# Kernel tuning notes

Hardware: AMD Instinct MI355X
Metric: run time of the kernel (lower is better)

The kernel has to match this reference:

```python
import jax, jax.numpy as jnp
from jax import lax
import numpy as np

B = 1024
CH = 32          # decomp.channel
LEVEL = 3        # decomp.level
CTOT = CH * (LEVEL + 1)   # 128, ODE state dim == GRU input dim
T_POINTS = 96    # decomp.eval_time_points
PRED_LEN = 96
HID = 128


def _dopri5_traj(y0, ts, Wo, bo):
    """Fixed-grid Dormand-Prince 5(4) integration of dy/dt = tanh(y Wo^T + bo).
    y0: [B, CTOT]; ts: [T]. Returns trajectory [T, B, CTOT]."""
    f = lambda y: jnp.tanh(y @ Wo.T + bo)

    def step(y, dt):
        k1 = f(y)
        k2 = f(y + dt * (0.2 * k1))
        k3 = f(y + dt * (3.0 / 40 * k1 + 9.0 / 40 * k2))
        k4 = f(y + dt * (44.0 / 45 * k1 - 56.0 / 15 * k2 + 32.0 / 9 * k3))
        k5 = f(y + dt * (19372.0 / 6561 * k1 - 25360.0 / 2187 * k2 + 64448.0 / 6561 * k3 - 212.0 / 729 * k4))
        k6 = f(y + dt * (9017.0 / 3168 * k1 - 355.0 / 33 * k2 + 46732.0 / 5247 * k3 + 49.0 / 176 * k4 - 5103.0 / 18656 * k5))
        y_next = y + dt * (35.0 / 384 * k1 + 500.0 / 1113 * k3 + 125.0 / 192 * k4 - 2187.0 / 6784 * k5 + 11.0 / 84 * k6)
        return y_next, y_next

    _, ys = lax.scan(step, y0, ts[1:] - ts[:-1])
    return jnp.concatenate([y0[None], ys], axis=0)


def _gru_layer(xs, W_ih, W_hh, b_ih, b_hh):
    """PyTorch-semantics GRU layer. xs: [T, B, D] -> hidden states [T, B, H]."""
    gi = jnp.einsum('tbd,gd->tbg', xs, W_ih) + b_ih  # precompute input gates
    H = W_hh.shape[1]

    def cell(h, gi_t):
        gh = h @ W_hh.T + b_hh
        i_r, i_z, i_n = jnp.split(gi_t, 3, axis=-1)
        h_r, h_z, h_n = jnp.split(gh, 3, axis=-1)
        r = jax.nn.sigmoid(i_r + h_r)
        z = jax.nn.sigmoid(i_z + h_z)
        n = jnp.tanh(i_n + r * h_n)
        h_new = (1.0 - z) * n + z * h
        return h_new, h_new

    h0 = jnp.zeros((xs.shape[1], H), xs.dtype)
    _, hs = lax.scan(cell, h0, gi)
    return hs


def setup_inputs() -> dict:
    key = jax.random.key(0)
    ks = jax.random.split(key, 20)
    s = 0.08  # ~1/sqrt(128), keeps GRU/ODE in a stable regime
    return {
        'x': jax.random.normal(ks[0], (B, CH, 256), jnp.float32),
        'yl': jax.random.normal(ks[1], (B, CH, 1), jnp.float32),
        'yh': jax.random.normal(ks[2], (B, CH * LEVEL, 1), jnp.float32),
        'W_ode': jax.random.normal(ks[3], (CTOT, CTOT), jnp.float32) * 0.05,
        'b_ode': jax.random.normal(ks[4], (CTOT,), jnp.float32) * 0.05,
        'W_ih0': jax.random.normal(ks[5], (3 * HID, CTOT), jnp.float32) * s,
        'W_hh0': jax.random.normal(ks[6], (3 * HID, HID), jnp.float32) * s,
        'b_ih0': jax.random.normal(ks[7], (3 * HID,), jnp.float32) * s,
        'b_hh0': jax.random.normal(ks[8], (3 * HID,), jnp.float32) * s,
        'W_ih1': jax.random.normal(ks[9], (3 * HID, HID), jnp.float32) * s,
        'W_hh1': jax.random.normal(ks[10], (3 * HID, HID), jnp.float32) * s,
        'b_ih1': jax.random.normal(ks[11], (3 * HID,), jnp.float32) * s,
        'b_hh1': jax.random.normal(ks[12], (3 * HID,), jnp.float32) * s,
        'W1': jax.random.normal(ks[13], (64, HID), jnp.float32) * s,
        'b1': jax.random.normal(ks[14], (64,), jnp.float32) * s,
        'W2': jax.random.normal(ks[15], (PRED_LEN * CH, 64), jnp.float32) * 0.125,
        'b2': jax.random.normal(ks[16], (PRED_LEN * CH,), jnp.float32) * 0.125,
    }


def reference(x, yl, yh, W_ode, b_ode,
              W_ih0, W_hh0, b_ih0, b_hh0,
              W_ih1, W_hh1, b_ih1, b_hh1,
              W1, b1, W2, b2):
    # coeffs = cat([yl] + yh, dim=1) -> [B, CTOT, 1] -> squeeze coeff length (=1)
    coeffs = jnp.concatenate([yl, yh], axis=1)[..., 0]  # [B, CTOT]
    ts = jnp.linspace(0.0, 1.0, T_POINTS)
    traj = _dopri5_traj(coeffs, ts, W_ode, b_ode)  # [T, B, CTOT]
    # rearrange 't b c l -> b t (c l)' with l == 1; GRU scans over leading T axis
    h1 = _gru_layer(traj, W_ih0, W_hh0, b_ih0, b_hh0)   # [T, B, HID]
    h2 = _gru_layer(h1, W_ih1, W_hh1, b_ih1, b_hh1)     # [T, B, HID]
    last = h2[-1]                                        # [B, HID]
    hidden = jax.nn.gelu(last @ W1.T + b1, approximate=False)
    pred = hidden @ W2.T + b2                            # [B, PRED_LEN*CH]
    return pred.reshape(-1, CH, PRED_LEN)
```

## Files before the change

### kernel.cpp

```cpp
#include <hip/hip_runtime.h>
#include <hip/hip_bf16.h>
#include <math.h>

#define ROWS 16
#define NTHR 512
#define TPTS 96
#define CTOT 128
#define NBLK 64

typedef __bf16 bf16x8_t __attribute__((ext_vector_type(8)));
typedef float f32x4_t __attribute__((ext_vector_type(4)));
typedef unsigned short us8_t __attribute__((ext_vector_type(8)));

__device__ __forceinline__ unsigned short f2b(float f) {
    union { float f; unsigned int i; } v; v.f = f;
    unsigned int r = v.i + 0x7fffu + ((v.i >> 16) & 1u);
    return (unsigned short)(r >> 16);
}
__device__ __forceinline__ f32x4_t mfma16(bf16x8_t a, bf16x8_t b, f32x4_t c) {
    return __builtin_amdgcn_mfma_f32_16x16x32_bf16(a, b, c, 0, 0, 0);
}
__device__ __forceinline__ bf16x8_t ldfrag(const unsigned short* p) {
    us8_t v = *(const us8_t*)p;
    return __builtin_bit_cast(bf16x8_t, v);
}
__device__ __forceinline__ bf16x8_t ldfrag_f32(const float* p) {
    bf16x8_t r;
#pragma unroll
    for (int j = 0; j < 8; ++j) {
        unsigned short us = f2b(p[j]);
        r[j] = __builtin_bit_cast(__bf16, us);
    }
    return r;
}
__device__ __forceinline__ float tanh_fast(float x) {
    float xc = fminf(fmaxf(x, -20.f), 20.f);
    float ez = __expf(-2.f * xc);
    return __fdividef(1.f - ez, 1.f + ez);
}
__device__ __forceinline__ float sigm(float x) {
    return __fdividef(1.f, 1.f + __expf(-x));
}

__global__ void __launch_bounds__(NTHR)
ode_forecaster(const float* __restrict__ yl,
               const float* __restrict__ yh,
               const float* __restrict__ Wode,
               const float* __restrict__ bode,
               const float* __restrict__ Wih0,
               const float* __restrict__ Whh0,
               const float* __restrict__ bih0,
               const float* __restrict__ bhh0,
               const float* __restrict__ Wih1,
               const float* __restrict__ Whh1,
               const float* __restrict__ bih1,
               const float* __restrict__ bhh1,
               const float* __restrict__ W1v,
               const float* __restrict__ b1v,
               const float* __restrict__ W2v,
               const float* __restrict__ b2v,
               float* __restrict__ outp,
               unsigned short* __restrict__ traj)
{
    const int tid  = threadIdx.x;
    const int lane = tid & 63;
    const int wv   = tid >> 6;
    const int l15  = lane & 15;
    const int quad = lane >> 4;
    const int r0   = blockIdx.x * ROWS;
    const int row0 = quad * 4;
    const int u    = wv * 16 + l15;

    __shared__ __align__(16) unsigned short hbuf[2][ROWS * 136];
    __shared__ __align__(16) unsigned short hidbuf[ROWS * 72];

    unsigned short* trajB = traj + (size_t)blockIdx.x * (TPTS * ROWS * CTOT);

    float y[4];
#pragma unroll
    for (int i = 0; i < 4; ++i) {
        int R = r0 + row0 + i;
        y[i] = (u < 32) ? yl[R * 32 + u] : yh[R * 96 + (u - 32)];
        unsigned short yb = f2b(y[i]);
        hbuf[0][(row0 + i) * 136 + u] = yb;
        trajB[(size_t)0 + (row0 + i) * CTOT + u] = yb;
    }

    bf16x8_t wode[4];
#pragma unroll
    for (int kt = 0; kt < 4; ++kt)
        wode[kt] = ldfrag_f32(Wode + u * 128 + kt * 32 + quad * 8);
    const float bo = bode[u];

    __syncthreads();

    const float dt = 1.0f / 95.0f;
    const float DA1_0 = 0.2f;
    const float DA2_0 = 3.f / 40.f, DA2_1 = 9.f / 40.f;
    const float DA3_0 = 44.f / 45.f, DA3_1 = -56.f / 15.f, DA3_2 = 32.f / 9.f;
    const float DA4_0 = 19372.f / 6561.f, DA4_1 = -25360.f / 2187.f,
                DA4_2 = 64448.f / 6561.f, DA4_3 = -212.f / 729.f;
    const float DA5_0 = 9017.f / 3168.f, DA5_1 = -355.f / 33.f,
                DA5_2 = 46732.f / 5247.f, DA5_3 = 49.f / 176.f, DA5_4 = -5103.f / 18656.f;
    const float B1 = 35.f / 384.f, B3 = 500.f / 1113.f, B4 = 125.f / 192.f,
                B5 = -2187.f / 6784.f, B6 = 11.f / 84.f;

    int p = 0;
    float kr[6][4];
#pragma unroll 1
    for (int t = 0; t < 95; ++t) {
#pragma unroll
        for (int s = 0; s < 6; ++s) {
            bf16x8_t af[4];
#pragma unroll
            for (int kt = 0; kt < 4; ++kt)
                af[kt] = ldfrag(&hbuf[p][l15 * 136 + kt * 32 + quad * 8]);
            f32x4_t acc = {0.f, 0.f, 0.f, 0.f};
#pragma unroll
            for (int kt = 0; kt < 4; ++kt) acc = mfma16(af[kt], wode[kt], acc);
#pragma unroll
            for (int i = 0; i < 4; ++i) kr[s][i] = tanh_fast(acc[i] + bo);

            if (s < 5) {
#pragma unroll
                for (int i = 0; i < 4; ++i) {
                    float zv = 0.f;
                    if (s == 0) { zv = DA1_0 * kr[0][i]; }
                    else if (s == 1) { zv = DA2_0 * kr[0][i] + DA2_1 * kr[1][i]; }
                    else if (s == 2) { zv = DA3_0 * kr[0][i] + DA3_1 * kr[1][i] + DA3_2 * kr[2][i]; }
                    else if (s == 3) { zv = DA4_0 * kr[0][i] + DA4_1 * kr[1][i] + DA4_2 * kr[2][i] + DA4_3 * kr[3][i]; }
                    else { zv = DA5_0 * kr[0][i] + DA5_1 * kr[1][i] + DA5_2 * kr[2][i] + DA5_3 * kr[3][i] + DA5_4 * kr[4][i]; }
                    hbuf[p ^ 1][(row0 + i) * 136 + u] = f2b(y[i] + dt * zv);
                }
            } else {
#pragma unroll
                for (int i = 0; i < 4; ++i) {
                    float fc = B1 * kr[0][i] + B3 * kr[2][i] + B4 * kr[3][i] + B5 * kr[4][i] + B6 * kr[5][i];
                    y[i] += dt * fc;
                    unsigned short yb = f2b(y[i]);
                    hbuf[p ^ 1][(row0 + i) * 136 + u] = yb;
                    trajB[(size_t)(t + 1) * (ROWS * CTOT) + (row0 + i) * CTOT + u] = yb;
                }
            }
            __syncthreads();
            p ^= 1;
        }
    }

    const float* WihL[2] = {Wih0, Wih1};
    const float* WhhL[2] = {Whh0, Whh1};
    const float* bihL[2] = {bih0, bih1};
    const float* bhhL[2] = {bhh0, bhh1};

    float h[4];
#pragma unroll 1
    for (int layer = 0; layer < 2; ++layer) {
        const float* Wih = WihL[layer];
        const float* Whh = WhhL[layer];
        bf16x8_t wih[3][4], whh[3][4];
#pragma unroll
        for (int g = 0; g < 3; ++g) {
            int nrow = g * 128 + u;
#pragma unroll
            for (int kt = 0; kt < 4; ++kt) {
                wih[g][kt] = ldfrag_f32(Wih + nrow * 128 + kt * 32 + quad * 8);
                whh[g][kt] = ldfrag_f32(Whh + nrow * 128 + kt * 32 + quad * 8);
            }
        }
        const float bir  = bihL[layer][u];
        const float biz  = bihL[layer][128 + u];
        const float bin_ = bihL[layer][256 + u];
        const float bhr  = bhhL[layer][u];
        const float bhz  = bhhL[layer][128 + u];
        const float bhn  = bhhL[layer][256 + u];

#pragma unroll
        for (int i = 0; i < 4; ++i) h[i] = 0.f;
        p = 0;
        for (int idx = tid; idx < ROWS * 136; idx += NTHR) hbuf[0][idx] = 0;
        __syncthreads();

#pragma unroll 1
        for (int t = 0; t < TPTS; ++t) {
            if (layer == 0 && t > 0) {
#pragma unroll
                for (int i = 0; i < 4; ++i)
                    trajB[(size_t)(t - 1) * (ROWS * CTOT) + (row0 + i) * CTOT + u] = f2b(h[i]);
            }
            const unsigned short* xp = trajB + (size_t)t * (ROWS * CTOT) + l15 * CTOT;
            bf16x8_t ax[4], ah[4];
#pragma unroll
            for (int kt = 0; kt < 4; ++kt) ax[kt] = ldfrag(xp + kt * 32 + quad * 8);
#pragma unroll
            for (int kt = 0; kt < 4; ++kt)
                ah[kt] = ldfrag(&hbuf[p][l15 * 136 + kt * 32 + quad * 8]);

            f32x4_t gi0 = {0.f,0.f,0.f,0.f}, gi1 = {0.f,0.f,0.f,0.f}, gi2 = {0.f,0.f,0.f,0.f};
            f32x4_t gh0 = {0.f,0.f,0.f,0.f}, gh1 = {0.f,0.f,0.f,0.f}, gh2 = {0.f,0.f,0.f,0.f};
#pragma unroll
            for (int kt = 0; kt < 4; ++kt) {
                gi0 = mfma16(ax[kt], wih[0][kt], gi0);
                gi1 = mfma16(ax[kt], wih[1][kt], gi1);
                gi2 = mfma16(ax[kt], wih[2][kt], gi2);
                gh0 = mfma16(ah[kt], whh[0][kt], gh0);
                gh1 = mfma16(ah[kt], whh[1][kt], gh1);
                gh2 = mfma16(ah[kt], whh[2][kt], gh2);
            }
#pragma unroll
            for (int i = 0; i < 4; ++i) {
                float rr = sigm((gi0[i] + bir) + (gh0[i] + bhr));
                float zz = sigm((gi1[i] + biz) + (gh1[i] + bhz));
                float nn = tanh_fast((gi2[i] + bin_) + rr * (gh2[i] + bhn));
                h[i] = (1.f - zz) * nn + zz * h[i];
                hbuf[p ^ 1][(row0 + i) * 136 + u] = f2b(h[i]);
            }
            __syncthreads();
            p ^= 1;
        }
        if (layer == 0) {
#pragma unroll
            for (int i = 0; i < 4; ++i)
                trajB[(size_t)95 * (ROWS * CTOT) + (row0 + i) * CTOT + u] = f2b(h[i]);
        }
    }

    if (wv < 4) {
        bf16x8_t a4[4], bw[4];
#pragma unroll
        for (int kt = 0; kt < 4; ++kt) {
            a4[kt] = ldfrag(&hbuf[p][l15 * 136 + kt * 32 + quad * 8]);
            bw[kt] = ldfrag_f32(W1v + (wv * 16 + l15) * 128 + kt * 32 + quad * 8);
        }
        f32x4_t acc = {0.f, 0.f, 0.f, 0.f};
#pragma unroll
        for (int kt = 0; kt < 4; ++kt) acc = mfma16(a4[kt], bw[kt], acc);
        const float bb = b1v[wv * 16 + l15];
#pragma unroll
        for (int i = 0; i < 4; ++i) {
            float x = acc[i] + bb;
            float g = 0.5f * x * (1.0f + erff(x * 0.70710678118654752f));
            hidbuf[(row0 + i) * 72 + wv * 16 + l15] = f2b(g);
        }
    }
    __syncthreads();

    bf16x8_t ahid[2];
#pragma unroll
    for (int kt = 0; kt < 2; ++kt)
        ahid[kt] = ldfrag(&hidbuf[l15 * 72 + kt * 32 + quad * 8]);
#pragma unroll 1
    for (int j = 0; j < 24; ++j) {
        int n = (wv * 24 + j) * 16 + l15;
        bf16x8_t bb0 = ldfrag_f32(W2v + n * 64 + quad * 8);
        bf16x8_t bb1 = ldfrag_f32(W2v + n * 64 + 32 + quad * 8);
        f32x4_t acc = {0.f, 0.f, 0.f, 0.f};
        acc = mfma16(ahid[0], bb0, acc);
        acc = mfma16(ahid[1], bb1, acc);
        const float bv = b2v[n];
#pragma unroll
        for (int i = 0; i < 4; ++i)
            outp[(size_t)(r0 + row0 + i) * 3072 + n] = acc[i] + bv;
    }
}

extern "C" void kernel_launch(void* const* d_in, const int* in_sizes, int n_in,
                              void* d_out, int out_size, void* d_ws, size_t ws_size,
                              hipStream_t stream) {
    const float* yl   = (const float*)d_in[1];
    const float* yh   = (const float*)d_in[2];
    const float* Wode = (const float*)d_in[3];
    const float* bode = (const float*)d_in[4];
    const float* Wih0 = (const float*)d_in[5];
    const float* Whh0 = (const float*)d_in[6];
    const float* bih0 = (const float*)d_in[7];
    const float* bhh0 = (const float*)d_in[8];
    const float* Wih1 = (const float*)d_in[9];
    const float* Whh1 = (const float*)d_in[10];
    const float* bih1 = (const float*)d_in[11];
    const float* bhh1 = (const float*)d_in[12];
    const float* W1v  = (const float*)d_in[13];
    const float* b1v  = (const float*)d_in[14];
    const float* W2v  = (const float*)d_in[15];
    const float* b2v  = (const float*)d_in[16];

    ode_forecaster<<<dim3(NBLK), dim3(NTHR), 0, stream>>>(
        yl, yh, Wode, bode, Wih0, Whh0, bih0, bhh0,
        Wih1, Whh1, bih1, bhh1, W1v, b1v, W2v, b2v,
        (float*)d_out, (unsigned short*)d_ws);
}
```

Measured before the change: 834.2 us.

## Split fused ODE-GRU kernel into ODE, input-gate GEMM, and recurrent GRU kernels

The single fused kernel is replaced by five launches. An ODE kernel processes 32 rows per block, a fully parallel kernel precomputes the GRU input gates for all timesteps, and a recurrent GRU kernel handles only the hidden-to-hidden matmul, prefetching gate values two steps ahead. This takes the input projection off the serial critical path and gives each block two independent MFMA chains. The cost is halving the recurrent grid to 32 blocks, which leaves most of the GPU idle, plus large global workspace traffic for the bf16-packed gate tensors. It also adds packed bf16 conversions, vectorized loads and a cheaper tanh.

```diff
diff --git a/kernel.cpp b/kernel.cpp
--- a/kernel.cpp
+++ b/kernel.cpp
@@ -2,11 +2,9 @@
 #include <hip/hip_bf16.h>
 #include <math.h>
 
-#define ROWS 16
-#define NTHR 512
 #define TPTS 96
 #define CTOT 128
-#define NBLK 64
+#define LDP 134
 
 typedef __bf16 bf16x8_t __attribute__((ext_vector_type(8)));
 typedef float f32x4_t __attribute__((ext_vector_type(4)));
@@ -17,6 +15,24 @@
     unsigned int r = v.i + 0x7fffu + ((v.i >> 16) & 1u);
     return (unsigned short)(r >> 16);
 }
+__device__ __forceinline__ unsigned int packbf2(float a, float b) {
+#if __has_builtin(__builtin_amdgcn_cvt_pk_bf16_f32)
+    typedef __bf16 bf16x2_t __attribute__((ext_vector_type(2)));
+    bf16x2_t v = __builtin_amdgcn_cvt_pk_bf16_f32(a, b);
+    return __builtin_bit_cast(unsigned int, v);
+#else
+    return (unsigned int)f2b(a) | ((unsigned int)f2b(b) << 16);
+#endif
+}
+__device__ __forceinline__ uint2 pack4(float v0, float v1, float v2, float v3) {
+    uint2 w; w.x = packbf2(v0, v1); w.y = packbf2(v2, v3); return w;
+}
+__device__ __forceinline__ float u2f_lo(unsigned int w) {
+    union { unsigned int i; float f; } v; v.i = w << 16; return v.f;
+}
+__device__ __forceinline__ float u2f_hi(unsigned int w) {
+    union { unsigned int i; float f; } v; v.i = w & 0xffff0000u; return v.f;
+}
 __device__ __forceinline__ f32x4_t mfma16(bf16x8_t a, bf16x8_t b, f32x4_t c) {
     return __builtin_amdgcn_mfma_f32_16x16x32_bf16(a, b, c, 0, 0, 0);
 }
@@ -24,242 +40,317 @@
     us8_t v = *(const us8_t*)p;
     return __builtin_bit_cast(bf16x8_t, v);
 }
-__device__ __forceinline__ bf16x8_t ldfrag_f32(const float* p) {
+__device__ __forceinline__ bf16x8_t ldfragW(const float* p) {
+    float4 a = *(const float4*)p;
+    float4 b = *(const float4*)(p + 4);
     bf16x8_t r;
-#pragma unroll
-    for (int j = 0; j < 8; ++j) {
-        unsigned short us = f2b(p[j]);
-        r[j] = __builtin_bit_cast(__bf16, us);
-    }
+    r[0] = __builtin_bit_cast(__bf16, f2b(a.x)); r[1] = __builtin_bit_cast(__bf16, f2b(a.y));
+    r[2] = __builtin_bit_cast(__bf16, f2b(a.z)); r[3] = __builtin_bit_cast(__bf16, f2b(a.w));
+    r[4] = __builtin_bit_cast(__bf16, f2b(b.x)); r[5] = __builtin_bit_cast(__bf16, f2b(b.y));
+    r[6] = __builtin_bit_cast(__bf16, f2b(b.z)); r[7] = __builtin_bit_cast(__bf16, f2b(b.w));
     return r;
 }
-__device__ __forceinline__ float tanh_fast(float x) {
-    float xc = fminf(fmaxf(x, -20.f), 20.f);
-    float ez = __expf(-2.f * xc);
-    return __fdividef(1.f - ez, 1.f + ez);
+__device__ __forceinline__ float tanh2(float x) {
+    float e = __expf(x + x);
+    return 1.f - __fdividef(2.f, e + 1.f);
 }
 __device__ __forceinline__ float sigm(float x) {
     return __fdividef(1.f, 1.f + __expf(-x));
 }
 
-__global__ void __launch_bounds__(NTHR)
-ode_forecaster(const float* __restrict__ yl,
-               const float* __restrict__ yh,
-               const float* __restrict__ Wode,
-               const float* __restrict__ bode,
-               const float* __restrict__ Wih0,
-               const float* __restrict__ Whh0,
-               const float* __restrict__ bih0,
-               const float* __restrict__ bhh0,
-               const float* __restrict__ Wih1,
-               const float* __restrict__ Whh1,
-               const float* __restrict__ bih1,
-               const float* __restrict__ bhh1,
-               const float* __restrict__ W1v,
-               const float* __restrict__ b1v,
-               const float* __restrict__ W2v,
-               const float* __restrict__ b2v,
-               float* __restrict__ outp,
-               unsigned short* __restrict__ traj)
+__global__ void __launch_bounds__(512, 1)
+k_ode(const float* __restrict__ yl, const float* __restrict__ yh,
+      const float* __restrict__ Wode, const float* __restrict__ bode,
+      unsigned short* __restrict__ yTraj)
 {
-    const int tid  = threadIdx.x;
-    const int lane = tid & 63;
-    const int wv   = tid >> 6;
-    const int l15  = lane & 15;
-    const int quad = lane >> 4;
-    const int r0   = blockIdx.x * ROWS;
-    const int row0 = quad * 4;
-    const int u    = wv * 16 + l15;
-
-    __shared__ __align__(16) unsigned short hbuf[2][ROWS * 136];
-    __shared__ __align__(16) unsigned short hidbuf[ROWS * 72];
-
-    unsigned short* trajB = traj + (size_t)blockIdx.x * (TPTS * ROWS * CTOT);
-
-    float y[4];
-#pragma unroll
-    for (int i = 0; i < 4; ++i) {
-        int R = r0 + row0 + i;
-        y[i] = (u < 32) ? yl[R * 32 + u] : yh[R * 96 + (u - 32)];
-        unsigned short yb = f2b(y[i]);
-        hbuf[0][(row0 + i) * 136 + u] = yb;
-        trajB[(size_t)0 + (row0 + i) * CTOT + u] = yb;
-    }
+    const int tid = threadIdx.x, lane = tid & 63, wv = tid >> 6;
+    const int l15 = lane & 15, quad = lane >> 4;
+    const int fbase = wv * 16 + quad * 4;
+    const int rbase = blockIdx.x * 32;
+
+    __shared__ __align__(16) unsigned short zbuf[2][32][LDP];
 
     bf16x8_t wode[4];
 #pragma unroll
     for (int kt = 0; kt < 4; ++kt)
-        wode[kt] = ldfrag_f32(Wode + u * 128 + kt * 32 + quad * 8);
-    const float bo = bode[u];
-
+        wode[kt] = ldfragW(Wode + (wv * 16 + l15) * CTOT + kt * 32 + quad * 8);
+    float bo[4];
+    {
+        float4 b4 = *(const float4*)(bode + fbase);
+        bo[0] = b4.x; bo[1] = b4.y; bo[2] = b4.z; bo[3] = b4.w;
+    }
+
+    float yA[4], yB[4];
+    {
+        int rA = rbase + l15, rB = rbase + 16 + l15;
+#pragma unroll
+        for (int i = 0; i < 4; ++i) {
+            int f = fbase + i;
+            yA[i] = (f < 32) ? yl[rA * 32 + f] : yh[rA * 96 + (f - 32)];
+            yB[i] = (f < 32) ? yl[rB * 32 + f] : yh[rB * 96 + (f - 32)];
+        }
+        *(uint2*)&zbuf[0][l15][fbase]      = pack4(yA[0], yA[1], yA[2], yA[3]);
+        *(uint2*)&zbuf[0][16 + l15][fbase] = pack4(yB[0], yB[1], yB[2], yB[3]);
+        *(uint2*)(yTraj + ((size_t)rA) * CTOT + fbase) = pack4(yA[0], yA[1], yA[2], yA[3]);
+        *(uint2*)(yTraj + ((size_t)rB) * CTOT + fbase) = pack4(yB[0], yB[1], yB[2], yB[3]);
+    }
     __syncthreads();
 
     const float dt = 1.0f / 95.0f;
-    const float DA1_0 = 0.2f;
-    const float DA2_0 = 3.f / 40.f, DA2_1 = 9.f / 40.f;
-    const float DA3_0 = 44.f / 45.f, DA3_1 = -56.f / 15.f, DA3_2 = 32.f / 9.f;
-    const float DA4_0 = 19372.f / 6561.f, DA4_1 = -25360.f / 2187.f,
-                DA4_2 = 64448.f / 6561.f, DA4_3 = -212.f / 729.f;
-    const float DA5_0 = 9017.f / 3168.f, DA5_1 = -355.f / 33.f,
-                DA5_2 = 46732.f / 5247.f, DA5_3 = 49.f / 176.f, DA5_4 = -5103.f / 18656.f;
     const float B1 = 35.f / 384.f, B3 = 500.f / 1113.f, B4 = 125.f / 192.f,
                 B5 = -2187.f / 6784.f, B6 = 11.f / 84.f;
 
     int p = 0;
-    float kr[6][4];
+    float krA[6][4], krB[6][4];
 #pragma unroll 1
     for (int t = 0; t < 95; ++t) {
 #pragma unroll
         for (int s = 0; s < 6; ++s) {
-            bf16x8_t af[4];
-#pragma unroll
-            for (int kt = 0; kt < 4; ++kt)
-                af[kt] = ldfrag(&hbuf[p][l15 * 136 + kt * 32 + quad * 8]);
-            f32x4_t acc = {0.f, 0.f, 0.f, 0.f};
-#pragma unroll
-            for (int kt = 0; kt < 4; ++kt) acc = mfma16(af[kt], wode[kt], acc);
-#pragma unroll
-            for (int i = 0; i < 4; ++i) kr[s][i] = tanh_fast(acc[i] + bo);
-
+            bf16x8_t fA[4], fB[4];
+#pragma unroll
+            for (int kt = 0; kt < 4; ++kt) {
+                fA[kt] = ldfrag(&zbuf[p][l15][kt * 32 + quad * 8]);
+                fB[kt] = ldfrag(&zbuf[p][16 + l15][kt * 32 + quad * 8]);
+            }
+            f32x4_t aA = {0.f, 0.f, 0.f, 0.f}, aB = {0.f, 0.f, 0.f, 0.f};
+#pragma unroll
+            for (int kt = 0; kt < 4; ++kt) {
+                aA = mfma16(wode[kt], fA[kt], aA);
+                aB = mfma16(wode[kt], fB[kt], aB);
+            }
+#pragma unroll
+            for (int i = 0; i < 4; ++i) {
+                krA[s][i] = tanh2(aA[i] + bo[i]);
+                krB[s][i] = tanh2(aB[i] + bo[i]);
+            }
             if (s < 5) {
+                float zA[4], zB[4];
 #pragma unroll
                 for (int i = 0; i < 4; ++i) {
-                    float zv = 0.f;
-                    if (s == 0) { zv = DA1_0 * kr[0][i]; }
-                    else if (s == 1) { zv = DA2_0 * kr[0][i] + DA2_1 * kr[1][i]; }
-                    else if (s == 2) { zv = DA3_0 * kr[0][i] + DA3_1 * kr[1][i] + DA3_2 * kr[2][i]; }
-                    else if (s == 3) { zv = DA4_0 * kr[0][i] + DA4_1 * kr[1][i] + DA4_2 * kr[2][i] + DA4_3 * kr[3][i]; }
-                    else { zv = DA5_0 * kr[0][i] + DA5_1 * kr[1][i] + DA5_2 * kr[2][i] + DA5_3 * kr[3][i] + DA5_4 * kr[4][i]; }
-                    hbuf[p ^ 1][(row0 + i) * 136 + u] = f2b(y[i] + dt * zv);
+                    float zvA, zvB;
+                    if (s == 0) {
+                        zvA = 0.2f * krA[0][i]; zvB = 0.2f * krB[0][i];
+                    } else if (s == 1) {
+                        zvA = (3.f/40.f)*krA[0][i] + (9.f/40.f)*krA[1][i];
+                        zvB = (3.f/40.f)*krB[0][i] + (9.f/40.f)*krB[1][i];
+                    } else if (s == 2) {
+                        zvA = (44.f/45.f)*krA[0][i] + (-56.f/15.f)*krA[1][i] + (32.f/9.f)*krA[2][i];
+                        zvB = (44.f/45.f)*krB[0][i] + (-56.f/15.f)*krB[1][i] + (32.f/9.f)*krB[2][i];
+                    } else if (s == 3) {
+                        zvA = (19372.f/6561.f)*krA[0][i] + (-25360.f/2187.f)*krA[1][i]
+                            + (64448.f/6561.f)*krA[2][i] + (-212.f/729.f)*krA[3][i];
+                        zvB = (19372.f/6561.f)*krB[0][i] + (-25360.f/2187.f)*krB[1][i]
+                            + (64448.f/6561.f)*krB[2][i] + (-212.f/729.f)*krB[3][i];
+                    } else {
+                        zvA = (9017.f/3168.f)*krA[0][i] + (-355.f/33.f)*krA[1][i]
+                            + (46732.f/5247.f)*krA[2][i] + (49.f/176.f)*krA[3][i]
+                            + (-5103.f/18656.f)*krA[4][i];
+                        zvB = (9017.f/3168.f)*krB[0][i] + (-355.f/33.f)*krB[1][i]
+                            + (46732.f/5247.f)*krB[2][i] + (49.f/176.f)*krB[3][i]
+                            + (-5103.f/18656.f)*krB[4][i];
+                    }
+                    zA[i] = yA[i] + dt * zvA; zB[i] = yB[i] + dt * zvB;
                 }
+                *(uint2*)&zbuf[p ^ 1][l15][fbase]      = pack4(zA[0], zA[1], zA[2], zA[3]);
+                *(uint2*)&zbuf[p ^ 1][16 + l15][fbase] = pack4(zB[0], zB[1], zB[2], zB[3]);
             } else {
 #pragma unroll
                 for (int i = 0; i < 4; ++i) {
-                    float fc = B1 * kr[0][i] + B3 * kr[2][i] + B4 * kr[3][i] + B5 * kr[4][i] + B6 * kr[5][i];
-                    y[i] += dt * fc;
-                    unsigned short yb = f2b(y[i]);
-                    hbuf[p ^ 1][(row0 + i) * 136 + u] = yb;
-                    trajB[(size_t)(t + 1) * (ROWS * CTOT) + (row0 + i) * CTOT + u] = yb;
+                    yA[i] += dt * (B1*krA[0][i] + B3*krA[2][i] + B4*krA[3][i] + B5*krA[4][i] + B6*krA[5][i]);
+                    yB[i] += dt * (B1*krB[0][i] + B3*krB[2][i] + B4*krB[3][i] + B5*krB[4][i] + B6*krB[5][i]);
                 }
+                uint2 pA = pack4(yA[0], yA[1], yA[2], yA[3]);
+                uint2 pB = pack4(yB[0], yB[1], yB[2], yB[3]);
+                *(uint2*)&zbuf[p ^ 1][l15][fbase]      = pA;
+                *(uint2*)&zbuf[p ^ 1][16 + l15][fbase] = pB;
+                *(uint2*)(yTraj + ((size_t)(t + 1) * 1024 + rbase + l15) * CTOT + fbase) = pA;
+                *(uint2*)(yTraj + ((size_t)(t + 1) * 1024 + rbase + 16 + l15) * CTOT + fbase) = pB;
             }
             __syncthreads();
             p ^= 1;
         }
     }
-
-    const float* WihL[2] = {Wih0, Wih1};
-    const float* WhhL[2] = {Whh0, Whh1};
-    const float* bihL[2] = {bih0, bih1};
-    const float* bhhL[2] = {bhh0, bhh1};
-
-    float h[4];
+}
+
+__global__ void __launch_bounds__(512, 1)
+k_gates(const float* __restrict__ W, const unsigned short* __restrict__ src,
+        uint2* __restrict__ gi)
+{
+    const int tid = threadIdx.x, lane = tid & 63, wv = tid >> 6;
+    const int l15 = lane & 15, quad = lane >> 4;
+    const int t = blockIdx.x >> 6, rt = blockIdx.x & 63;
+
+    const unsigned short* xp = src + ((size_t)t * 1024 + rt * 16 + l15) * CTOT;
+    bf16x8_t bf[4];
+#pragma unroll
+    for (int kt = 0; kt < 4; ++kt) bf[kt] = ldfrag(xp + kt * 32 + quad * 8);
+#pragma unroll
+    for (int g = 0; g < 3; ++g) {
+        bf16x8_t wf[4];
+#pragma unroll
+        for (int kt = 0; kt < 4; ++kt)
+            wf[kt] = ldfragW(W + (size_t)(g * 128 + wv * 16 + l15) * CTOT + kt * 32 + quad * 8);
+        f32x4_t a = {0.f, 0.f, 0.f, 0.f};
+#pragma unroll
+        for (int kt = 0; kt < 4; ++kt) a = mfma16(wf[kt], bf[kt], a);
+        gi[((size_t)(t * 64 + rt) * 24 + wv * 3 + g) * 64 + lane] = pack4(a[0], a[1], a[2], a[3]);
+    }
+}
+
+__global__ void __launch_bounds__(512, 1)
+k_gru(const float* __restrict__ Whh, const float* __restrict__ bih, const float* __restrict__ bhh,
+      const uint2* __restrict__ gi, unsigned short* __restrict__ outTraj,
+      const float* __restrict__ W1v, const float* __restrict__ b1v,
+      const float* __restrict__ W2v, const float* __restrict__ b2v,
+      float* __restrict__ outp, int doHead)
+{
+    const int tid = threadIdx.x, lane = tid & 63, wv = tid >> 6;
+    const int l15 = lane & 15, quad = lane >> 4;
+    const int fbase = wv * 16 + quad * 4;
+    const int rbase = blockIdx.x * 32;
+    const int rtA = blockIdx.x * 2, rtB = rtA + 1;
+
+    __shared__ __align__(16) unsigned short zbuf[2][32][LDP];
+    __shared__ __align__(16) unsigned short hidbuf[32][72];
+
+    bf16x8_t whh[3][4];
+#pragma unroll
+    for (int g = 0; g < 3; ++g)
+#pragma unroll
+        for (int kt = 0; kt < 4; ++kt)
+            whh[g][kt] = ldfragW(Whh + (size_t)(g * 128 + wv * 16 + l15) * CTOT + kt * 32 + quad * 8);
+    float bi[3][4], bh[3][4];
+#pragma unroll
+    for (int g = 0; g < 3; ++g) {
+        float4 a = *(const float4*)(bih + g * 128 + fbase);
+        float4 b = *(const float4*)(bhh + g * 128 + fbase);
+        bi[g][0] = a.x; bi[g][1] = a.y; bi[g][2] = a.z; bi[g][3] = a.w;
+        bh[g][0] = b.x; bh[g][1] = b.y; bh[g][2] = b.z; bh[g][3] = b.w;
+    }
+
+    float hA[4] = {0.f, 0.f, 0.f, 0.f}, hB[4] = {0.f, 0.f, 0.f, 0.f};
+    *(uint2*)&zbuf[0][l15][fbase]      = pack4(0.f, 0.f, 0.f, 0.f);
+    *(uint2*)&zbuf[0][16 + l15][fbase] = pack4(0.f, 0.f, 0.f, 0.f);
+    __syncthreads();
+
+#define GIX(t, rt, g) (((size_t)((t) * 64 + (rt)) * 24 + wv * 3 + (g)) * 64 + lane)
+    uint2 a0[3], a1[3], a2[3], b0[3], b1[3], b2[3];
+#pragma unroll
+    for (int g = 0; g < 3; ++g) {
+        a0[g] = gi[GIX(0, rtA, g)]; a1[g] = gi[GIX(1, rtA, g)];
+        b0[g] = gi[GIX(0, rtB, g)]; b1[g] = gi[GIX(1, rtB, g)];
+    }
+
+    int p = 0;
 #pragma unroll 1
-    for (int layer = 0; layer < 2; ++layer) {
-        const float* Wih = WihL[layer];
-        const float* Whh = WhhL[layer];
-        bf16x8_t wih[3][4], whh[3][4];
+    for (int t = 0; t < TPTS; ++t) {
+        if (t + 2 < TPTS) {
+#pragma unroll
+            for (int g = 0; g < 3; ++g) {
+                a2[g] = gi[GIX(t + 2, rtA, g)];
+                b2[g] = gi[GIX(t + 2, rtB, g)];
+            }
+        }
+        bf16x8_t fA[4], fB[4];
+#pragma unroll
+        for (int kt = 0; kt < 4; ++kt) {
+            fA[kt] = ldfrag(&zbuf[p][l15][kt * 32 + quad * 8]);
+            fB[kt] = ldfrag(&zbuf[p][16 + l15][kt * 32 + quad * 8]);
+        }
+        f32x4_t gA[3], gB[3];
 #pragma unroll
         for (int g = 0; g < 3; ++g) {
-            int nrow = g * 128 + u;
-#pragma unroll
-            for (int kt = 0; kt < 4; ++kt) {
-                wih[g][kt] = ldfrag_f32(Wih + nrow * 128 + kt * 32 + quad * 8);
-                whh[g][kt] = ldfrag_f32(Whh + nrow * 128 + kt * 32 + quad * 8);
-            }
-        }
-        const float bir  = bihL[layer][u];
-        const float biz  = bihL[layer][128 + u];
-        const float bin_ = bihL[layer][256 + u];
-        const float bhr  = bhhL[layer][u];
-        const float bhz  = bhhL[layer][128 + u];
-        const float bhn  = bhhL[layer][256 + u];
-
-#pragma unroll
-        for (int i = 0; i < 4; ++i) h[i] = 0.f;
-        p = 0;
-        for (int idx = tid; idx < ROWS * 136; idx += NTHR) hbuf[0][idx] = 0;
+            gA[g] = (f32x4_t){0.f, 0.f, 0.f, 0.f};
+            gB[g] = (f32x4_t){0.f, 0.f, 0.f, 0.f};
+        }
+#pragma unroll
+        for (int kt = 0; kt < 4; ++kt) {
+            gA[0] = mfma16(whh[0][kt], fA[kt], gA[0]);
+            gB[0] = mfma16(whh[0][kt], fB[kt], gB[0]);
+            gA[1] = mfma16(whh[1][kt], fA[kt], gA[1]);
+            gB[1] = mfma16(whh[1][kt], fB[kt], gB[1]);
+            gA[2] = mfma16(whh[2][kt], fA[kt], gA[2]);
+            gB[2] = mfma16(whh[2][kt], fB[kt], gB[2]);
+        }
+        float grA[3][4], grB[3][4];
+#pragma unroll
+        for (int g = 0; g < 3; ++g) {
+            grA[g][0] = u2f_lo(a0[g].x); grA[g][1] = u2f_hi(a0[g].x);
+            grA[g][2] = u2f_lo(a0[g].y); grA[g][3] = u2f_hi(a0[g].y);
+            grB[g][0] = u2f_lo(b0[g].x); grB[g][1] = u2f_hi(b0[g].x);
+            grB[g][2] = u2f_lo(b0[g].y); grB[g][3] = u2f_hi(b0[g].y);
+        }
+#pragma unroll
+        for (int i = 0; i < 4; ++i) {
+            float rA = sigm((grA[0][i] + bi[0][i]) + (gA[0][i] + bh[0][i]));
+            float zA = sigm((grA[1][i] + bi[1][i]) + (gA[1][i] + bh[1][i]));
+            float nA = tanh2((grA[2][i] + bi[2][i]) + rA * (gA[2][i] + bh[2][i]));
+            hA[i] = (1.f - zA) * nA + zA * hA[i];
+            float rB = sigm((grB[0][i] + bi[0][i]) + (gB[0][i] + bh[0][i]));
+            float zB = sigm((grB[1][i] + bi[1][i]) + (gB[1][i] + bh[1][i]));
+            float nB = tanh2((grB[2][i] + bi[2][i]) + rB * (gB[2][i] + bh[2][i]));
+            hB[i] = (1.f - zB) * nB + zB * hB[i];
+        }
+        uint2 pA = pack4(hA[0], hA[1], hA[2], hA[3]);
+        uint2 pB = pack4(hB[0], hB[1], hB[2], hB[3]);
+        *(uint2*)&zbuf[p ^ 1][l15][fbase]      = pA;
+        *(uint2*)&zbuf[p ^ 1][16 + l15][fbase] = pB;
+        if (outTraj) {
+            *(uint2*)(outTraj + ((size_t)t * 1024 + rbase + l15) * CTOT + fbase)      = pA;
+            *(uint2*)(outTraj + ((size_t)t * 1024 + rbase + 16 + l15) * CTOT + fbase) = pB;
+        }
         __syncthreads();
-
+        p ^= 1;
+#pragma unroll
+        for (int g = 0; g < 3; ++g) { a0[g] = a1[g]; a1[g] = a2[g]; b0[g] = b1[g]; b1[g] = b2[g]; }
+    }
+#undef GIX
+
+    if (doHead) {
+        int grp = wv >> 2, mt = wv & 3;
+        int lrow = grp * 16 + l15;
+        bf16x8_t wf[4], hf[4];
+#pragma unroll
+        for (int kt = 0; kt < 4; ++kt) {
+            wf[kt] = ldfragW(W1v + (size_t)(mt * 16 + l15) * CTOT + kt * 32 + quad * 8);
+            hf[kt] = ldfrag(&zbuf[p][lrow][kt * 32 + quad * 8]);
+        }
+        f32x4_t acc = {0.f, 0.f, 0.f, 0.f};
+#pragma unroll
+        for (int kt = 0; kt < 4; ++kt) acc = mfma16(wf[kt], hf[kt], acc);
+        float4 bb = *(const float4*)(b1v + mt * 16 + quad * 4);
+        const float* bbp = (const float*)&bb;
+        float gl[4];
+#pragma unroll
+        for (int i = 0; i < 4; ++i) {
+            float x = acc[i] + bbp[i];
+            gl[i] = 0.5f * x * (1.0f + erff(x * 0.70710678118654752f));
+        }
+        *(uint2*)&hidbuf[lrow][mt * 16 + quad * 4] = pack4(gl[0], gl[1], gl[2], gl[3]);
+        __syncthreads();
+
+        bf16x8_t hdA[2], hdB[2];
+#pragma unroll
+        for (int kt = 0; kt < 2; ++kt) {
+            hdA[kt] = ldfrag(&hidbuf[l15][kt * 32 + quad * 8]);
+            hdB[kt] = ldfrag(&hidbuf[16 + l15][kt * 32 + quad * 8]);
+        }
 #pragma unroll 1
-        for (int t = 0; t < TPTS; ++t) {
-            if (layer == 0 && t > 0) {
-#pragma unroll
-                for (int i = 0; i < 4; ++i)
-                    trajB[(size_t)(t - 1) * (ROWS * CTOT) + (row0 + i) * CTOT + u] = f2b(h[i]);
-            }
-            const unsigned short* xp = trajB + (size_t)t * (ROWS * CTOT) + l15 * CTOT;
-            bf16x8_t ax[4], ah[4];
-#pragma unroll
-            for (int kt = 0; kt < 4; ++kt) ax[kt] = ldfrag(xp + kt * 32 + quad * 8);
-#pragma unroll
-            for (int kt = 0; kt < 4; ++kt)
-                ah[kt] = ldfrag(&hbuf[p][l15 * 136 + kt * 32 + quad * 8]);
-
-            f32x4_t gi0 = {0.f,0.f,0.f,0.f}, gi1 = {0.f,0.f,0.f,0.f}, gi2 = {0.f,0.f,0.f,0.f};
-            f32x4_t gh0 = {0.f,0.f,0.f,0.f}, gh1 = {0.f,0.f,0.f,0.f}, gh2 = {0.f,0.f,0.f,0.f};
-#pragma unroll
-            for (int kt = 0; kt < 4; ++kt) {
-                gi0 = mfma16(ax[kt], wih[0][kt], gi0);
-                gi1 = mfma16(ax[kt], wih[1][kt], gi1);
-                gi2 = mfma16(ax[kt], wih[2][kt], gi2);
-                gh0 = mfma16(ah[kt], whh[0][kt], gh0);
-                gh1 = mfma16(ah[kt], whh[1][kt], gh1);
-                gh2 = mfma16(ah[kt], whh[2][kt], gh2);
-            }
-#pragma unroll
-            for (int i = 0; i < 4; ++i) {
-                float rr = sigm((gi0[i] + bir) + (gh0[i] + bhr));
-                float zz = sigm((gi1[i] + biz) + (gh1[i] + bhz));
-                float nn = tanh_fast((gi2[i] + bin_) + rr * (gh2[i] + bhn));
-                h[i] = (1.f - zz) * nn + zz * h[i];
-                hbuf[p ^ 1][(row0 + i) * 136 + u] = f2b(h[i]);
-            }
-            __syncthreads();
-            p ^= 1;
-        }
-        if (layer == 0) {
-#pragma unroll
-            for (int i = 0; i < 4; ++i)
-                trajB[(size_t)95 * (ROWS * CTOT) + (row0 + i) * CTOT + u] = f2b(h[i]);
-        }
-    }
-
-    if (wv < 4) {
-        bf16x8_t a4[4], bw[4];
-#pragma unroll
-        for (int kt = 0; kt < 4; ++kt) {
-            a4[kt] = ldfrag(&hbuf[p][l15 * 136 + kt * 32 + quad * 8]);
-            bw[kt] = ldfrag_f32(W1v + (wv * 16 + l15) * 128 + kt * 32 + quad * 8);
-        }
-        f32x4_t acc = {0.f, 0.f, 0.f, 0.f};
-#pragma unroll
-        for (int kt = 0; kt < 4; ++kt) acc = mfma16(a4[kt], bw[kt], acc);
-        const float bb = b1v[wv * 16 + l15];
-#pragma unroll
-        for (int i = 0; i < 4; ++i) {
-            float x = acc[i] + bb;
-            float g = 0.5f * x * (1.0f + erff(x * 0.70710678118654752f));
-            hidbuf[(row0 + i) * 72 + wv * 16 + l15] = f2b(g);
-        }
-    }
-    __syncthreads();
-
-    bf16x8_t ahid[2];
-#pragma unroll
-    for (int kt = 0; kt < 2; ++kt)
-        ahid[kt] = ldfrag(&hidbuf[l15 * 72 + kt * 32 + quad * 8]);
-#pragma unroll 1
-    for (int j = 0; j < 24; ++j) {
-        int n = (wv * 24 + j) * 16 + l15;
-        bf16x8_t bb0 = ldfrag_f32(W2v + n * 64 + quad * 8);
-        bf16x8_t bb1 = ldfrag_f32(W2v + n * 64 + 32 + quad * 8);
-        f32x4_t acc = {0.f, 0.f, 0.f, 0.f};
-        acc = mfma16(ahid[0], bb0, acc);
-        acc = mfma16(ahid[1], bb1, acc);
-        const float bv = b2v[n];
-#pragma unroll
-        for (int i = 0; i < 4; ++i)
-            outp[(size_t)(r0 + row0 + i) * 3072 + n] = acc[i] + bv;
+        for (int j = 0; j < 24; ++j) {
+            int mt2 = wv * 24 + j;
+            bf16x8_t wf0 = ldfragW(W2v + (size_t)(mt2 * 16 + l15) * 64 + quad * 8);
+            bf16x8_t wf1 = ldfragW(W2v + (size_t)(mt2 * 16 + l15) * 64 + 32 + quad * 8);
+            float4 bv = *(const float4*)(b2v + mt2 * 16 + quad * 4);
+            const float* bvp = (const float*)&bv;
+            f32x4_t aA = {0.f, 0.f, 0.f, 0.f}, aB = {0.f, 0.f, 0.f, 0.f};
+            aA = mfma16(wf0, hdA[0], aA); aA = mfma16(wf1, hdA[1], aA);
+            aB = mfma16(wf0, hdB[0], aB); aB = mfma16(wf1, hdB[1], aB);
+            float4 oA, oB;
+            oA.x = aA[0] + bvp[0]; oA.y = aA[1] + bvp[1]; oA.z = aA[2] + bvp[2]; oA.w = aA[3] + bvp[3];
+            oB.x = aB[0] + bvp[0]; oB.y = aB[1] + bvp[1]; oB.z = aB[2] + bvp[2]; oB.w = aB[3] + bvp[3];
+            *(float4*)(outp + (size_t)(rbase + l15) * 3072 + mt2 * 16 + quad * 4) = oA;
+            *(float4*)(outp + (size_t)(rbase + 16 + l15) * 3072 + mt2 * 16 + quad * 4) = oB;
+        }
     }
 }
 
@@ -282,9 +373,19 @@
     const float* b1v  = (const float*)d_in[14];
     const float* W2v  = (const float*)d_in[15];
     const float* b2v  = (const float*)d_in[16];
-
-    ode_forecaster<<<dim3(NBLK), dim3(NTHR), 0, stream>>>(
-        yl, yh, Wode, bode, Wih0, Whh0, bih0, bhh0,
-        Wih1, Whh1, bih1, bhh1, W1v, b1v, W2v, b2v,
-        (float*)d_out, (unsigned short*)d_ws);
-}
+    float* outp = (float*)d_out;
+
+    char* wsb = (char*)d_ws;
+    unsigned short* yTraj  = (unsigned short*)(wsb);
+    unsigned short* h1Traj = (unsigned short*)(wsb + 25165824);
+    uint2* gi0 = (uint2*)(wsb + 2 * 25165824);
+    uint2* gi1 = (uint2*)(wsb + 2 * 25165824 + 75497472);
+
+    k_ode<<<dim3(32), dim3(512), 0, stream>>>(yl, yh, Wode, bode, yTraj);
+    k_gates<<<dim3(96 * 64), dim3(512), 0, stream>>>(Wih0, yTraj, gi0);
+    k_gru<<<dim3(32), dim3(512), 0, stream>>>(Whh0, bih0, bhh0, gi0, h1Traj,
+                                              W1v, b1v, W2v, b2v, outp, 0);
+    k_gates<<<dim3(96 * 64), dim3(512), 0, stream>>>(Wih1, h1Traj, gi1);
+    k_gru<<<dim3(32), dim3(512), 0, stream>>>(Whh1, bih1, bhh1, gi1, nullptr,
+                                              W1v, b1v, W2v, b2v, outp, 1);
+}
```

Measured after the change: 2.351 ms. 182% more time.
